# Kernel tuning notes

Hardware: AMD Instinct MI355X
Metric: run time of the kernel (lower is better)

Reference implementation:

```python
import jax, jax.numpy as jnp
import numpy as np

N = 262144
H = 512
NUM_SEGMENTS = 64

def setup_inputs() -> dict:
    key = jax.random.key(0)
    k1, k2, k3, k4 = jax.random.split(key, 4)
    h_V = jax.random.normal(k1, (N, H), dtype=jnp.float32)
    batch_id = jnp.sort(jax.random.randint(k2, (N,), 0, NUM_SEGMENTS))
    scale = 1.0 / np.sqrt(H)
    W1 = jax.random.normal(k3, (H, H), dtype=jnp.float32) * scale
    b1 = jnp.zeros((H,), dtype=jnp.float32)
    W2 = jax.random.normal(k4, (H, H), dtype=jnp.float32) * scale
    b2 = jnp.zeros((H,), dtype=jnp.float32)
    return {"h_V": h_V, "batch_id": batch_id, "W1": W1, "b1": b1, "W2": W2, "b2": b2}

def reference(h_V, batch_id, W1, b1, W2, b2):
    # scatter_mean over segments: [S, H]
    seg_sum = jax.ops.segment_sum(h_V, batch_id, num_segments=NUM_SEGMENTS)
    counts = jax.ops.segment_sum(jnp.ones((h_V.shape[0],), h_V.dtype), batch_id,
                                 num_segments=NUM_SEGMENTS)
    c_V = seg_sum / jnp.maximum(counts, 1.0)[:, None]
    # gated MLP on per-segment context (nn.Linear: x @ W.T + b)
    hdn = jax.nn.relu(c_V @ W1.T + b1)
    gate = jax.nn.sigmoid(hdn @ W2.T + b2)  # [S, H]
    # gather back to nodes and gate
    return h_V * gate[batch_id]
```

## Files before the change

kernel.cpp:

```cpp
#include <hip/hip_runtime.h>

#define H 512
#define NSEG 64
#define CHUNK 256

typedef float f4 __attribute__((ext_vector_type(4)));

__device__ __forceinline__ f4 ntload4(const f4* p) {
    return __builtin_nontemporal_load(p);
}
__device__ __forceinline__ void ntstore4(f4* p, f4 v) {
    __builtin_nontemporal_store(v, p);
}

__global__ __launch_bounds__(512) void k_segsum(
    const f4* __restrict__ hv, const int* __restrict__ bid,
    float* __restrict__ seg_sum, int* __restrict__ counts)
{
    __shared__ int sb[CHUNK];
    const int base = blockIdx.x * CHUNK;
    const int tid  = threadIdx.x;
    if (tid < CHUNK) sb[tid] = bid[base + tid];
    __syncthreads();

    const int g = tid >> 7;
    const int q = tid & 127;

    f4 acc = (f4)(0.f);
    int cur = sb[g];
    int cnt = 0;

    for (int i = 0; i < 64; i += 2) {
        const int r0 = g + (i << 2);
        const int r1 = r0 + 4;
        const f4 v0 = ntload4(hv + (size_t)(base + r0) * (H / 4) + q);
        const f4 v1 = ntload4(hv + (size_t)(base + r1) * (H / 4) + q);
        const int s0 = sb[r0];
        const int s1 = sb[r1];
        if (s0 != cur) {
            float* dst = seg_sum + cur * H + q * 4;
            atomicAdd(dst + 0, acc[0]); atomicAdd(dst + 1, acc[1]);
            atomicAdd(dst + 2, acc[2]); atomicAdd(dst + 3, acc[3]);
            if (q == 0) atomicAdd(counts + cur, cnt);
            acc = (f4)(0.f); cnt = 0; cur = s0;
        }
        acc += v0; ++cnt;
        if (s1 != cur) {
            float* dst = seg_sum + cur * H + q * 4;
            atomicAdd(dst + 0, acc[0]); atomicAdd(dst + 1, acc[1]);
            atomicAdd(dst + 2, acc[2]); atomicAdd(dst + 3, acc[3]);
            if (q == 0) atomicAdd(counts + cur, cnt);
            acc = (f4)(0.f); cnt = 0; cur = s1;
        }
        acc += v1; ++cnt;
    }
    float* dst = seg_sum + cur * H + q * 4;
    atomicAdd(dst + 0, acc[0]); atomicAdd(dst + 1, acc[1]);
    atomicAdd(dst + 2, acc[2]); atomicAdd(dst + 3, acc[3]);
    if (q == 0) atomicAdd(counts + cur, cnt);
}

__global__ __launch_bounds__(512) void k_mlp(
    const float* __restrict__ seg_sum, const int* __restrict__ counts,
    const float* __restrict__ W1, const float* __restrict__ b1,
    const float* __restrict__ W2, const float* __restrict__ b2,
    float* __restrict__ gate)
{
    __shared__ float c[H];
    __shared__ float hd[H];
    const int s   = blockIdx.x;
    const int tid = threadIdx.x;

    const float cntf = fmaxf((float)counts[s], 1.0f);
    c[tid] = seg_sum[s * H + tid] / cntf;
    __syncthreads();

    const int w = tid >> 6;
    const int l = tid & 63;

    for (int jb = 0; jb < H / 8; ++jb) {
        const int j = jb * 8 + w;
        const float* __restrict__ wr = W1 + (size_t)j * H;
        float acc = 0.f;
        #pragma unroll
        for (int m = 0; m < H / 64; ++m)
            acc += c[m * 64 + l] * wr[m * 64 + l];
        #pragma unroll
        for (int off = 32; off > 0; off >>= 1)
            acc += __shfl_xor(acc, off, 64);
        if (l == 0) hd[j] = fmaxf(acc + b1[j], 0.f);
    }
    __syncthreads();

    for (int jb = 0; jb < H / 8; ++jb) {
        const int j = jb * 8 + w;
        const float* __restrict__ wr = W2 + (size_t)j * H;
        float acc = 0.f;
        #pragma unroll
        for (int m = 0; m < H / 64; ++m)
            acc += hd[m * 64 + l] * wr[m * 64 + l];
        #pragma unroll
        for (int off = 32; off > 0; off >>= 1)
            acc += __shfl_xor(acc, off, 64);
        if (l == 0) gate[s * H + j] = 1.0f / (1.0f + expf(-(acc + b2[j])));
    }
}

__global__ __launch_bounds__(512) void k_gate(
    const f4* __restrict__ hv, const int* __restrict__ bid,
    const f4* __restrict__ gate, f4* __restrict__ out)
{
    __shared__ int sb[CHUNK];
    const int base = blockIdx.x * CHUNK;
    const int tid  = threadIdx.x;
    if (tid < CHUNK) sb[tid] = bid[base + tid];
    __syncthreads();

    const int g = tid >> 7;
    const int q = tid & 127;

    int cur = sb[g];
    f4 gv = gate[(size_t)cur * (H / 4) + q];

    for (int i = 0; i < 64; i += 2) {
        const int r0 = g + (i << 2);
        const int r1 = r0 + 4;
        const f4 v0 = ntload4(hv + (size_t)(base + r0) * (H / 4) + q);
        const f4 v1 = ntload4(hv + (size_t)(base + r1) * (H / 4) + q);
        const int s0 = sb[r0];
        const int s1 = sb[r1];
        if (s0 != cur) { cur = s0; gv = gate[(size_t)cur * (H / 4) + q]; }
        ntstore4(out + (size_t)(base + r0) * (H / 4) + q, v0 * gv);
        if (s1 != cur) { cur = s1; gv = gate[(size_t)cur * (H / 4) + q]; }
        ntstore4(out + (size_t)(base + r1) * (H / 4) + q, v1 * gv);
    }
}

extern "C" void kernel_launch(void* const* d_in, const int* in_sizes, int n_in,
                              void* d_out, int out_size, void* d_ws, size_t ws_size,
                              hipStream_t stream)
{
    const float* h_V      = (const float*)d_in[0];
    const int*   batch_id = (const int*)d_in[1];
    const float* W1       = (const float*)d_in[2];
    const float* b1       = (const float*)d_in[3];
    const float* W2       = (const float*)d_in[4];
    const float* b2       = (const float*)d_in[5];

    const int N = in_sizes[0] / H;

    char*  ws       = (char*)d_ws;
    float* seg_sum  = (float*)ws;
    int*   counts   = (int*)(ws + 131072);
    float* gate     = (float*)(ws + 131072 + 256);

    hipMemsetAsync(d_ws, 0, 131072 + 256, stream);

    k_segsum<<<N / CHUNK, 512, 0, stream>>>(
        (const f4*)h_V, batch_id, seg_sum, counts);

    k_mlp<<<NSEG, 512, 0, stream>>>(seg_sum, counts, W1, b1, W2, b2, gate);

    k_gate<<<N / CHUNK, 512, 0, stream>>>(
        (const f4*)h_V, batch_id, (const f4*)gate, (f4*)d_out);
}
```

Measured before the change: 397.1 us.

## Add uniform-segment fast paths, drop nontemporal loads, reverse gate block order

Adds a fast path in both the segment-sum and gate kernels for chunks whose rows all belong to one segment. There the sum uses four independent accumulators with a shared-memory reduction and a single set of atomics per block, and the gate kernel skips per-row segment checks. The h_V loads switch from nontemporal to regular loads, and the gate kernel walks blocks in reverse order. Together these aim to reuse the tail of h_V still in the large last-level cache from the first pass, reducing HBM reads. The cost is extra code paths and shared memory.

```diff
diff --git a/kernel.cpp b/kernel.cpp
--- a/kernel.cpp
+++ b/kernel.cpp
@@ -3,12 +3,10 @@
 #define H 512
 #define NSEG 64
 #define CHUNK 256
+#define QV (H / 4)
 
 typedef float f4 __attribute__((ext_vector_type(4)));
 
-__device__ __forceinline__ f4 ntload4(const f4* p) {
-    return __builtin_nontemporal_load(p);
-}
 __device__ __forceinline__ void ntstore4(f4* p, f4 v) {
     __builtin_nontemporal_store(v, p);
 }
@@ -18,6 +16,7 @@
     float* __restrict__ seg_sum, int* __restrict__ counts)
 {
     __shared__ int sb[CHUNK];
+    __shared__ f4 sred[4][QV];
     const int base = blockIdx.x * CHUNK;
     const int tid  = threadIdx.x;
     if (tid < CHUNK) sb[tid] = bid[base + tid];
@@ -26,33 +25,45 @@
     const int g = tid >> 7;
     const int q = tid & 127;
 
+    if (sb[0] == sb[CHUNK - 1]) {
+        const int seg = sb[0];
+        const f4* p = hv + (size_t)(base + g) * QV + q;
+        f4 a0 = (f4)(0.f), a1 = (f4)(0.f), a2 = (f4)(0.f), a3 = (f4)(0.f);
+        for (int i = 0; i < 16; ++i) {
+            const size_t o = (size_t)i * (16 * QV);
+            const f4 v0 = p[o];
+            const f4 v1 = p[o + 4 * QV];
+            const f4 v2 = p[o + 8 * QV];
+            const f4 v3 = p[o + 12 * QV];
+            a0 += v0; a1 += v1; a2 += v2; a3 += v3;
+        }
+        sred[g][q] = (a0 + a1) + (a2 + a3);
+        __syncthreads();
+        if (g == 0) {
+            const f4 t = sred[0][q] + sred[1][q] + sred[2][q] + sred[3][q];
+            float* dst = seg_sum + seg * H + q * 4;
+            atomicAdd(dst + 0, t[0]); atomicAdd(dst + 1, t[1]);
+            atomicAdd(dst + 2, t[2]); atomicAdd(dst + 3, t[3]);
+            if (q == 0) atomicAdd(counts + seg, CHUNK);
+        }
+        return;
+    }
+
     f4 acc = (f4)(0.f);
     int cur = sb[g];
     int cnt = 0;
-
-    for (int i = 0; i < 64; i += 2) {
-        const int r0 = g + (i << 2);
-        const int r1 = r0 + 4;
-        const f4 v0 = ntload4(hv + (size_t)(base + r0) * (H / 4) + q);
-        const f4 v1 = ntload4(hv + (size_t)(base + r1) * (H / 4) + q);
-        const int s0 = sb[r0];
-        const int s1 = sb[r1];
-        if (s0 != cur) {
+    for (int i = 0; i < 64; ++i) {
+        const int r = g + (i << 2);
+        const f4 v = hv[(size_t)(base + r) * QV + q];
+        const int s = sb[r];
+        if (s != cur) {
             float* dst = seg_sum + cur * H + q * 4;
             atomicAdd(dst + 0, acc[0]); atomicAdd(dst + 1, acc[1]);
             atomicAdd(dst + 2, acc[2]); atomicAdd(dst + 3, acc[3]);
             if (q == 0) atomicAdd(counts + cur, cnt);
-            acc = (f4)(0.f); cnt = 0; cur = s0;
+            acc = (f4)(0.f); cnt = 0; cur = s;
         }
-        acc += v0; ++cnt;
-        if (s1 != cur) {
-            float* dst = seg_sum + cur * H + q * 4;
-            atomicAdd(dst + 0, acc[0]); atomicAdd(dst + 1, acc[1]);
-            atomicAdd(dst + 2, acc[2]); atomicAdd(dst + 3, acc[3]);
-            if (q == 0) atomicAdd(counts + cur, cnt);
-            acc = (f4)(0.f); cnt = 0; cur = s1;
-        }
-        acc += v1; ++cnt;
+        acc += v; ++cnt;
     }
     float* dst = seg_sum + cur * H + q * 4;
     atomicAdd(dst + 0, acc[0]); atomicAdd(dst + 1, acc[1]);
@@ -111,7 +122,8 @@
     const f4* __restrict__ gate, f4* __restrict__ out)
 {
     __shared__ int sb[CHUNK];
-    const int base = blockIdx.x * CHUNK;
+    const int blk  = gridDim.x - 1 - blockIdx.x;
+    const int base = blk * CHUNK;
     const int tid  = threadIdx.x;
     if (tid < CHUNK) sb[tid] = bid[base + tid];
     __syncthreads();
@@ -119,20 +131,32 @@
     const int g = tid >> 7;
     const int q = tid & 127;
 
+    if (sb[0] == sb[CHUNK - 1]) {
+        const f4 gv = gate[(size_t)sb[0] * QV + q];
+        const f4* p = hv  + (size_t)(base + g) * QV + q;
+        f4*       o = out + (size_t)(base + g) * QV + q;
+        for (int i = 0; i < 16; ++i) {
+            const size_t off = (size_t)i * (16 * QV);
+            const f4 v0 = p[off];
+            const f4 v1 = p[off + 4 * QV];
+            const f4 v2 = p[off + 8 * QV];
+            const f4 v3 = p[off + 12 * QV];
+            ntstore4(o + off,           v0 * gv);
+            ntstore4(o + off + 4 * QV,  v1 * gv);
+            ntstore4(o + off + 8 * QV,  v2 * gv);
+            ntstore4(o + off + 12 * QV, v3 * gv);
+        }
+        return;
+    }
+
     int cur = sb[g];
-    f4 gv = gate[(size_t)cur * (H / 4) + q];
-
-    for (int i = 0; i < 64; i += 2) {
-        const int r0 = g + (i << 2);
-        const int r1 = r0 + 4;
-        const f4 v0 = ntload4(hv + (size_t)(base + r0) * (H / 4) + q);
-        const f4 v1 = ntload4(hv + (size_t)(base + r1) * (H / 4) + q);
-        const int s0 = sb[r0];
-        const int s1 = sb[r1];
-        if (s0 != cur) { cur = s0; gv = gate[(size_t)cur * (H / 4) + q]; }
-        ntstore4(out + (size_t)(base + r0) * (H / 4) + q, v0 * gv);
-        if (s1 != cur) { cur = s1; gv = gate[(size_t)cur * (H / 4) + q]; }
-        ntstore4(out + (size_t)(base + r1) * (H / 4) + q, v1 * gv);
+    f4 gv = gate[(size_t)cur * QV + q];
+    for (int i = 0; i < 64; ++i) {
+        const int r = g + (i << 2);
+        const f4 v = hv[(size_t)(base + r) * QV + q];
+        const int s = sb[r];
+        if (s != cur) { cur = s; gv = gate[(size_t)cur * QV + q]; }
+        ntstore4(out + (size_t)(base + r) * QV + q, v * gv);
     }
 }
 
@@ -149,10 +173,10 @@
 
     const int N = in_sizes[0] / H;
 
-    char*  ws       = (char*)d_ws;
-    float* seg_sum  = (float*)ws;
-    int*   counts   = (int*)(ws + 131072);
-    float* gate     = (float*)(ws + 131072 + 256);
+    char*  ws      = (char*)d_ws;
+    float* seg_sum = (float*)ws;
+    int*   counts  = (int*)(ws + 131072);
+    float* gate    = (float*)(ws + 131072 + 256);
 
     hipMemsetAsync(d_ws, 0, 131072 + 256, stream);
 
```

New measurement: 400.5 us. No clear change (+0.9%).
